# Performance work log

Measured on AMD Instinct MI355X. Metric: run time of the kernel, lower is better.

Reference implementation:

```python
import jax, jax.numpy as jnp
import numpy as np
from jax import lax

B, H, W = 8, 500, 500
M = 2048          # per-image cap on active bottleneck voxels (ragged -> fixed)
GRID = 125        # bottleneck grid size
ENC_RANGE = 125.0
HEADS, ATTN_CH, CH = 4, 128, 64
EPS = 1e-5
NEG = -1e9

def _conv(x, w, b, stride, pad):
    y = lax.conv_general_dilated(x, w, (stride, stride), pad,
                                 dimension_numbers=('NCHW', 'HWIO', 'NCHW'))
    return y + b[None, :, None, None]

def _maxpool2(m):
    return lax.reduce_window(m, -jnp.inf, lax.max, (1, 1, 2, 2), (1, 1, 2, 2), 'VALID')

def setup_inputs():
    key = jax.random.key(0)
    ks = jax.random.split(key, 12)
    occ = (jax.random.uniform(ks[0], (B, 1, H, W)) < 0.005).astype(jnp.float32)
    x = jax.random.normal(ks[1], (B, 1, H, W), dtype=jnp.float32) * occ
    def rn(k, shape, scale):
        return jax.random.normal(k, shape, dtype=jnp.float32) * scale
    return {
        'x': x,
        'w0': rn(ks[2], (3, 3, 1, 32), 0.3), 'b0': jnp.zeros(32, jnp.float32),
        'g0': jnp.ones(32, jnp.float32), 'be0': jnp.zeros(32, jnp.float32),
        'w1': rn(ks[3], (2, 2, 32, 64), 0.1), 'b1': jnp.zeros(64, jnp.float32),
        'g1': jnp.ones(64, jnp.float32), 'be1': jnp.zeros(64, jnp.float32),
        'w2': rn(ks[4], (2, 2, 64, 64), 0.08), 'b2': jnp.zeros(64, jnp.float32),
        'g2': jnp.ones(64, jnp.float32), 'be2': jnp.zeros(64, jnp.float32),
        'wpe': rn(ks[5], (2, 2, CH), 0.5), 'bpe': jnp.zeros((2, CH), jnp.float32),
        'wq': rn(ks[6], (2, CH, ATTN_CH), 0.12), 'bq': jnp.zeros((2, ATTN_CH), jnp.float32),
        'wk': rn(ks[7], (2, CH, ATTN_CH), 0.12), 'bk': jnp.zeros((2, ATTN_CH), jnp.float32),
        'wv': rn(ks[8], (2, CH, ATTN_CH), 0.12), 'bv': jnp.zeros((2, ATTN_CH), jnp.float32),
        'wo': rn(ks[9], (2, ATTN_CH, CH), 0.09), 'bo': jnp.zeros((2, CH), jnp.float32),
        'wh': rn(ks[10], (CH, 4), 0.12), 'bh': jnp.zeros(4, jnp.float32),
    }

def reference(x, w0, b0, g0, be0, w1, b1, g1, be1, w2, b2, g2, be2,
              wpe, bpe, wq, bq, wk, bk, wv, bv, wo, bo, wh, bh):
    # active-site mask (Voxels.from_dense)
    mask0 = (x != 0).any(axis=1, keepdims=True).astype(x.dtype)   # [B,1,500,500]

    def bn_relu(y, g, be):
        # eval-mode BatchNorm1d over active voxel features (running stats 0/1)
        return jax.nn.relu(g[None, :, None, None] * y / jnp.sqrt(1.0 + EPS)
                           + be[None, :, None, None])

    # enc0: submanifold 3x3/s1 -> active set unchanged; inactive inputs are zero
    y = bn_relu(_conv(x, w0, b0, 1, 'SAME'), g0, be0) * mask0
    # enc1/enc2: strided 2x2/s2 -> output active iff any input in window active
    mask1 = _maxpool2(mask0)
    y = bn_relu(_conv(y, w1, b1, 2, 'VALID'), g1, be1) * mask1
    mask2 = _maxpool2(mask1)
    y = bn_relu(_conv(y, w2, b2, 2, 'VALID'), g2, be2) * mask2    # [B,64,125,125]

    # gather active bottleneck voxels per image (ragged -> fixed M + validity mask)
    mflat = mask2.reshape(B, GRID * GRID)
    vals, idx = lax.top_k(mflat, M)     # active-first; stable tie-break (lowest idx)
    valid = vals                        # [B,M] in {0,1}
    feats = jnp.take_along_axis(
        y.reshape(B, CH, GRID * GRID).transpose(0, 2, 1),
        idx[:, :, None], axis=1)        # [B,M,64]
    pos = jnp.stack([idx // GRID, idx % GRID], axis=-1).astype(x.dtype) / ENC_RANGE

    dh = ATTN_CH // HEADS
    kmask = (1.0 - valid)[:, None, None, :] * NEG
    for i in range(2):  # N_ATTN structurally distinct layers
        pe = pos @ wpe[i] + bpe[i]
        h = feats + pe
        q = (h @ wq[i] + bq[i]).reshape(B, M, HEADS, dh)
        k = (h @ wk[i] + bk[i]).reshape(B, M, HEADS, dh)
        v = (h @ wv[i] + bv[i]).reshape(B, M, HEADS, dh)
        s = jnp.einsum('bqhd,bkhd->bhqk', q, k) / jnp.sqrt(jnp.asarray(dh, x.dtype))
        a = jax.nn.softmax(s + kmask, axis=-1)
        o = jnp.einsum('bhqk,bkhd->bqhd', a, v).reshape(B, M, ATTN_CH)
        feats = (feats + o @ wo[i] + bo[i]) * valid[..., None]

    # sparse_global_avg_pool: mean over active voxels per image
    counts = jnp.clip(valid.sum(axis=1, keepdims=True), 1.0, None)
    pooled = feats.sum(axis=1) / counts                            # [B,64]
    return pooled @ wh + bh                                        # [B,4]
```

## Files before the change

kernel.cpp:

```cpp
#include <hip/hip_runtime.h>

#define BDIM   8
#define NPIX   250000
#define G1N    62500
#define G2N    15625
#define NB0    977
#define NB1    245
#define NB2    62
#define CAP0   4096
#define CAP1   4096
#define CAPM   2048
#define CH     64
#define ACH    128
#define NHEADS 4
#define DH     32
#define KSPLIT 4

static constexpr float BN_INV    = 0.99999500003749969f;
static constexpr float ATT_SCALE = 0.17677669529663687f;

typedef _Float16 f16x8 __attribute__((ext_vector_type(8)));
typedef float f32x4 __attribute__((ext_vector_type(4)));

static constexpr size_t E_MAP0  = 0;
static constexpr size_t E_MAP1  = E_MAP0 + (size_t)BDIM*NPIX;
static constexpr size_t E_CNT   = E_MAP1 + (size_t)BDIM*G1N;
static constexpr size_t E_ZEND  = E_CNT + 32;
static constexpr size_t E_BC    = E_ZEND;
static constexpr size_t E_BO    = E_BC + (size_t)3*BDIM*1024;
static constexpr size_t E_BM    = E_BO + (size_t)3*BDIM*1024;
static constexpr size_t E_LIST0 = E_BM + (size_t)3*BDIM*1024*8;
static constexpr size_t E_LIST1 = E_LIST0 + (size_t)BDIM*CAP0;
static constexpr size_t E_LIST2 = E_LIST1 + (size_t)BDIM*CAP1;
static constexpr size_t E_Y0    = E_LIST2 + (size_t)BDIM*CAPM;
static constexpr size_t E_Y1    = E_Y0 + (size_t)BDIM*CAP0*32;
static constexpr size_t E_FE    = E_Y1 + (size_t)BDIM*CAP1*64;
static constexpr size_t E_QF    = E_FE + (size_t)BDIM*CAPM*64;
static constexpr size_t E_KF    = E_QF + (size_t)32*CAPM*32/2;
static constexpr size_t E_VT    = E_KF + (size_t)32*CAPM*32/2;
static constexpr size_t E_PACC  = E_VT + (size_t)32*CAPM*32/2;
static constexpr size_t E_PML   = E_PACC + (size_t)32*CAPM*KSPLIT*32;


__device__ __forceinline__ bool act0(const float* x, int pix, int b) {
  return (pix < NPIX) && (x[(size_t)b * NPIX + pix] != 0.f);
}
__device__ __forceinline__ bool act1(const int* map0, int p, int b) {
  if (p >= G1N) return false;
  int i = p / 250, j = p - i * 250;
  const int* m = map0 + (size_t)b * NPIX + (2 * i) * 500 + 2 * j;
  return (m[0] | m[1] | m[500] | m[501]) != 0;
}
__device__ __forceinline__ bool act2(const int* map1, int p, int b) {
  if (p >= G2N) return false;
  int i = p / 125, j = p - i * 125;
  const int* m = map1 + (size_t)b * G1N + (2 * i) * 250 + 2 * j;
  return (m[0] | m[1] | m[250] | m[251]) != 0;
}

#define COUNT_BODY(ACT_EXPR)                                            \
  int idx = blockIdx.x * 256 + threadIdx.x;                             \
  int b = blockIdx.y;                                                   \
  bool act = (ACT_EXPR);                                                \
  unsigned long long mask = __ballot(act);                              \
  __shared__ int wc[4];                                                 \
  if ((threadIdx.x & 63) == 0) {                                        \
    wc[threadIdx.x >> 6] = __popcll(mask);                              \
    bm[((size_t)b * 1024 + blockIdx.x) * 4 + (threadIdx.x >> 6)] = mask;\
  }                                                                     \
  __syncthreads();                                                      \
  if (threadIdx.x == 0)                                                 \
    bcnt[b * 1024 + blockIdx.x] = wc[0] + wc[1] + wc[2] + wc[3];

__global__ void k_cnt0(const float* __restrict__ x, int* __restrict__ bcnt,
                       unsigned long long* __restrict__ bm) {
  COUNT_BODY(act0(x, idx, b))
}
__global__ void k_cnt1(const int* __restrict__ map0, int* __restrict__ bcnt,
                       unsigned long long* __restrict__ bm) {
  COUNT_BODY(act1(map0, idx, b))
}
__global__ void k_cnt2(const int* __restrict__ map1, int* __restrict__ bcnt,
                       unsigned long long* __restrict__ bm) {
  COUNT_BODY(act2(map1, idx, b))
}

__global__ __launch_bounds__(256) void k_scan(const int* __restrict__ bcnt,
                                              int* __restrict__ boff,
                                              int* __restrict__ cnt,
                                              int nblk, int cbase) {
  int b = blockIdx.x;
  int t = threadIdx.x;
  int base = t * 4;
  int v[4];
  int ts = 0;
#pragma unroll
  for (int u = 0; u < 4; ++u) {
    v[u] = (base + u < nblk) ? bcnt[b * 1024 + base + u] : 0;
    ts += v[u];
  }
  int lane = t & 63, w = t >> 6;
  int incl = ts;
#pragma unroll
  for (int off = 1; off < 64; off <<= 1) {
    int o = __shfl_up(incl, off, 64);
    if (lane >= off) incl += o;
  }
  __shared__ int wsum[4];
  if (lane == 63) wsum[w] = incl;
  __syncthreads();
  int woff = 0;
#pragma unroll
  for (int k = 0; k < 3; ++k) if (k < w) woff += wsum[k];
  int run = woff + incl - ts;
#pragma unroll
  for (int u = 0; u < 4; ++u) {
    if (base + u < nblk) boff[b * 1024 + base + u] = run;
    run += v[u];
  }
  if (t == 255) cnt[cbase + b] = run;
}

#define EMIT_PROLOG                                                     \
  int idx = blockIdx.x * 256 + threadIdx.x;                             \
  int b = blockIdx.y;                                                   \
  int lane = threadIdx.x & 63;                                          \
  unsigned long long mask =                                             \
      bm[((size_t)b * 1024 + blockIdx.x) * 4 + (threadIdx.x >> 6)];     \
  bool act = (mask >> lane) & 1;                                        \
  __shared__ int wbase[4];                                              \
  if (lane == 0) wbase[threadIdx.x >> 6] = __popcll(mask);              \
  __syncthreads();                                                      \
  if (threadIdx.x == 0) {                                               \
    int s = boff[b * 1024 + blockIdx.x];                                \
    for (int w = 0; w < 4; ++w) { int c = wbase[w]; wbase[w] = s; s += c; } \
  }                                                                     \
  __syncthreads();                                                      \
  int slot = wbase[threadIdx.x >> 6] + __popcll(mask & ((1ull << lane) - 1ull));

__global__ void k_emit0(const unsigned long long* __restrict__ bm,
                        const int* __restrict__ boff,
                        int* __restrict__ map0, int* __restrict__ list0) {
  EMIT_PROLOG
  if (act && slot < CAP0) {
    list0[b * CAP0 + slot] = idx;
    map0[(size_t)b * NPIX + idx] = slot + 1;
  }
}
__global__ void k_emit1(const unsigned long long* __restrict__ bm,
                        const int* __restrict__ boff,
                        int* __restrict__ map1, int* __restrict__ list1) {
  EMIT_PROLOG
  if (act && slot < CAP1) {
    list1[b * CAP1 + slot] = idx;
    map1[(size_t)b * G1N + idx] = slot + 1;
  }
}
__global__ void k_emit2(const unsigned long long* __restrict__ bm,
                        const int* __restrict__ boff,
                        int* __restrict__ list2) {
  EMIT_PROLOG
  if (act && slot < CAPM) list2[b * CAPM + slot] = idx;
}


__global__ void k_y0(const float* __restrict__ x, const float* __restrict__ w0,
                     const float* __restrict__ b0, const float* __restrict__ g0,
                     const float* __restrict__ be0,
                     const int* __restrict__ list0, const int* __restrict__ cnt,
                     float* __restrict__ y0) {
  int t = blockIdx.x * 256 + threadIdx.x;
  int b = t >> 17;
  int r = t & 131071;
  int slot = r >> 5, c = r & 31;
  int n = min(cnt[b], CAP0);
  if (slot >= n) return;
  int pix = list0[b * CAP0 + slot];
  int i = pix / 500, j = pix - i * 500;
  float acc = b0[c];
#pragma unroll
  for (int di = 0; di < 3; ++di) {
    int ii = i + di - 1;
    if ((unsigned)ii >= 500u) continue;
#pragma unroll
    for (int dj = 0; dj < 3; ++dj) {
      int jj = j + dj - 1;
      if ((unsigned)jj >= 500u) continue;
      acc += x[(size_t)b * NPIX + ii * 500 + jj] * w0[(di * 3 + dj) * 32 + c];
    }
  }
  float o = g0[c] * acc * BN_INV + be0[c];
  y0[((size_t)(b * CAP0) + slot) * 32 + c] = fmaxf(o, 0.f);
}

__global__ void k_y1(const float* __restrict__ y0, const float* __restrict__ w1,
                     const float* __restrict__ b1, const float* __restrict__ g1,
                     const float* __restrict__ be1,
                     const int* __restrict__ map0, const int* __restrict__ list1,
                     const int* __restrict__ cnt, float* __restrict__ y1) {
  int b = blockIdx.x >> 9;
  int sblk = blockIdx.x & 511;
  int s0 = sblk * 8;
  int n = min(cnt[BDIM + b], CAP1);
  if (s0 >= n) return;
  __shared__ float inT[4][32][8];
  for (int idx = threadIdx.x; idx < 1024; idx += 64) {
    int s = idx & 7;
    int r = idx >> 3;
    int ci = r & 31, pp = r >> 5;
    float v = 0.f;
    int sg = s0 + s;
    if (sg < n) {
      int p = list1[b * CAP1 + sg];
      int i = p / 250, j = p - i * 250;
      int sm = map0[(size_t)b * NPIX + (2 * i + (pp >> 1)) * 500 + (2 * j + (pp & 1))];
      if (sm) v = y0[((size_t)(b * CAP0) + (sm - 1)) * 32 + ci];
    }
    inT[pp][ci][s] = v;
  }
  __syncthreads();
  int co = threadIdx.x;
  float acc[8];
#pragma unroll
  for (int s = 0; s < 8; ++s) acc[s] = b1[co];
#pragma unroll 2
  for (int pp = 0; pp < 4; ++pp)
    for (int ci = 0; ci < 32; ++ci) {
      float wv = w1[((pp << 5) + ci) * 64 + co];
      float4 i0 = *(const float4*)&inT[pp][ci][0];
      float4 i1 = *(const float4*)&inT[pp][ci][4];
      acc[0] += i0.x * wv; acc[1] += i0.y * wv; acc[2] += i0.z * wv; acc[3] += i0.w * wv;
      acc[4] += i1.x * wv; acc[5] += i1.y * wv; acc[6] += i1.z * wv; acc[7] += i1.w * wv;
    }
  int smax = min(8, n - s0);
  for (int s = 0; s < smax; ++s) {
    float o = g1[co] * acc[s] * BN_INV + be1[co];
    y1[((size_t)(b * CAP1) + s0 + s) * 64 + co] = fmaxf(o, 0.f);
  }
}

__global__ void k_y2(const float* __restrict__ y1, const float* __restrict__ w2,
                     const float* __restrict__ b2, const float* __restrict__ g2,
                     const float* __restrict__ be2,
                     const int* __restrict__ map1, const int* __restrict__ list2,
                     const int* __restrict__ cnt, float* __restrict__ feats) {
  int b = blockIdx.x >> 8;
  int sblk = blockIdx.x & 255;
  int s0 = sblk * 8;
  int n = min(cnt[2 * BDIM + b], CAPM);
  if (s0 >= n) return;
  __shared__ float inT[4][64][8];
  for (int idx = threadIdx.x; idx < 2048; idx += 64) {
    int s = idx & 7;
    int r = idx >> 3;
    int ci = r & 63, pp = r >> 6;
    float v = 0.f;
    int sg = s0 + s;
    if (sg < n) {
      int p = list2[b * CAPM + sg];
      int i = p / 125, j = p - i * 125;
      int sm = map1[(size_t)b * G1N + (2 * i + (pp >> 1)) * 250 + (2 * j + (pp & 1))];
      if (sm) v = y1[((size_t)(b * CAP1) + (sm - 1)) * 64 + ci];
    }
    inT[pp][ci][s] = v;
  }
  __syncthreads();
  int co = threadIdx.x;
  float acc[8];
#pragma unroll
  for (int s = 0; s < 8; ++s) acc[s] = b2[co];
#pragma unroll 2
  for (int pp = 0; pp < 4; ++pp)
    for (int ci = 0; ci < 64; ++ci) {
      float wv = w2[((pp << 6) + ci) * 64 + co];
      float4 i0 = *(const float4*)&inT[pp][ci][0];
      float4 i1 = *(const float4*)&inT[pp][ci][4];
      acc[0] += i0.x * wv; acc[1] += i0.y * wv; acc[2] += i0.z * wv; acc[3] += i0.w * wv;
      acc[4] += i1.x * wv; acc[5] += i1.y * wv; acc[6] += i1.z * wv; acc[7] += i1.w * wv;
    }
  int smax = min(8, n - s0);
  for (int s = 0; s < smax; ++s) {
    float o = g2[co] * acc[s] * BN_INV + be2[co];
    feats[((size_t)(b * CAPM) + s0 + s) * 64 + co] = fmaxf(o, 0.f);
  }
}


__global__ void k_qkv(const float* __restrict__ feats, const int* __restrict__ list2,
                      const int* __restrict__ cnt,
                      const float* __restrict__ wpe, const float* __restrict__ bpe,
                      const float* __restrict__ wq, const float* __restrict__ bq,
                      const float* __restrict__ wk, const float* __restrict__ bk,
                      const float* __restrict__ wv, const float* __restrict__ bv,
                      int layer, _Float16* __restrict__ qf, _Float16* __restrict__ kf,
                      _Float16* __restrict__ vt) {
  int b = blockIdx.x & 7;
  int sblk = blockIdx.x >> 3;
  int s0 = sblk * 8;
  int n = min(cnt[2 * BDIM + b], CAPM);
  if (s0 >= n) return;
  __shared__ float hT[64][8];
  for (int idx = threadIdx.x; idx < 512; idx += 128) {
    int s = idx & 7, c = idx >> 3;
    float hv = 0.f;
    int sg = s0 + s;
    if (sg < n) {
      int p = list2[b * CAPM + sg];
      int i = p / 125, j = p - i * 125;
      hv = feats[((size_t)(b * CAPM) + sg) * 64 + c]
         + (float)i * (1.f / 125.f) * wpe[(layer * 2 + 0) * 64 + c]
         + (float)j * (1.f / 125.f) * wpe[(layer * 2 + 1) * 64 + c]
         + bpe[layer * 64 + c];
    }
    hT[c][s] = hv;
  }
  __syncthreads();
  int o = threadIdx.x;
  float accq[8], acck[8], accv[8];
  float bqv = bq[layer * 128 + o], bkv = bk[layer * 128 + o], bvv = bv[layer * 128 + o];
#pragma unroll
  for (int s = 0; s < 8; ++s) { accq[s] = bqv; acck[s] = bkv; accv[s] = bvv; }
  const float* wq_ = wq + (size_t)layer * 64 * 128 + o;
  const float* wk_ = wk + (size_t)layer * 64 * 128 + o;
  const float* wv_ = wv + (size_t)layer * 64 * 128 + o;
  for (int c = 0; c < 64; ++c) {
    float wqv = wq_[c * 128], wkv = wk_[c * 128], wvv = wv_[c * 128];
    float4 h0 = *(const float4*)&hT[c][0];
    float4 h1 = *(const float4*)&hT[c][4];
    float hh[8] = {h0.x, h0.y, h0.z, h0.w, h1.x, h1.y, h1.z, h1.w};
#pragma unroll
    for (int s = 0; s < 8; ++s) {
      accq[s] += hh[s] * wqv; acck[s] += hh[s] * wkv; accv[s] += hh[s] * wvv;
    }
  }
  int hd = o >> 5, d = o & 31;
  size_t bh = (size_t)(b * NHEADS + hd);
  int smax = min(8, n - s0);
  for (int s = 0; s < smax; ++s) {
    size_t rb = (bh * CAPM + s0 + s) * 32 + d;
    qf[rb] = (_Float16)accq[s];
    kf[rb] = (_Float16)acck[s];
    vt[(bh * 32 + d) * CAPM + s0 + s] = (_Float16)accv[s];
  }
}


union U4H8 { uint4 u; f16x8 h; };
union PKU  { _Float16 h[2]; unsigned int u; };

#define LOADK(K0, K1, K2, K3, T0)                                          \
  K0 = *(const f16x8*)(kf + (bh + (T0) + qr) * 32 + g8);                   \
  K1 = *(const f16x8*)(kf + (bh + (T0) + 16 + qr) * 32 + g8);              \
  K2 = *(const f16x8*)(kf + (bh + (T0) + 32 + qr) * 32 + g8);              \
  K3 = *(const f16x8*)(kf + (bh + (T0) + 48 + qr) * 32 + g8);

#define LOADV(V0, V1, V2, V3, T0)                                          \
  V0 = *(const f16x8*)(vbase + (size_t)qr * CAPM + (T0) + g8);             \
  V1 = *(const f16x8*)(vbase + (size_t)(16 + qr) * CAPM + (T0) + g8);      \
  V2 = *(const f16x8*)(vbase + (size_t)qr * CAPM + (T0) + 32 + g8);        \
  V3 = *(const f16x8*)(vbase + (size_t)(16 + qr) * CAPM + (T0) + 32 + g8);

#define PROCESS(K0, K1, K2, K3, V0, V1, V2, V3, T0)                        \
  {                                                                        \
    f32x4 z = {0.f, 0.f, 0.f, 0.f};                                        \
    f32x4 st0 = __builtin_amdgcn_mfma_f32_16x16x32_f16(K0, fq, z, 0, 0, 0);\
    f32x4 st1 = __builtin_amdgcn_mfma_f32_16x16x32_f16(K1, fq, z, 0, 0, 0);\
    f32x4 st2 = __builtin_amdgcn_mfma_f32_16x16x32_f16(K2, fq, z, 0, 0, 0);\
    f32x4 st3 = __builtin_amdgcn_mfma_f32_16x16x32_f16(K3, fq, z, 0, 0, 0);\
    if ((T0) + 64 > n) {                                                   \
      _Pragma("unroll") for (int r = 0; r < 4; ++r) {                      \
        if ((T0) + 4 * g + r >= n)      st0[r] = -1e30f;                   \
        if ((T0) + 16 + 4 * g + r >= n) st1[r] = -1e30f;                   \
        if ((T0) + 32 + 4 * g + r >= n) st2[r] = -1e30f;                   \
        if ((T0) + 48 + 4 * g + r >= n) st3[r] = -1e30f;                   \
      }                                                                    \
    }                                                                      \
    float tm = st0[0];                                                     \
    _Pragma("unroll") for (int r = 1; r < 4; ++r) tm = fmaxf(tm, st0[r]);  \
    _Pragma("unroll") for (int r = 0; r < 4; ++r) tm = fmaxf(tm, st1[r]);  \
    _Pragma("unroll") for (int r = 0; r < 4; ++r) tm = fmaxf(tm, st2[r]);  \
    _Pragma("unroll") for (int r = 0; r < 4; ++r) tm = fmaxf(tm, st3[r]);  \
    tm = fmaxf(tm, __shfl_xor(tm, 16));                                    \
    tm = fmaxf(tm, __shfl_xor(tm, 32));                                    \
    float mn = fmaxf(m, tm * ATT_SCALE);                                   \
    float f_ = __expf(m - mn);                                             \
    m = mn;                                                                \
    float ls = 0.f;                                                        \
    {                                                                      \
      PKU a, c;                                                            \
      a.h[0] = (_Float16)__expf(st0[0] * ATT_SCALE - mn);                  \
      a.h[1] = (_Float16)__expf(st0[1] * ATT_SCALE - mn);                  \
      c.h[0] = (_Float16)__expf(st0[2] * ATT_SCALE - mn);                  \
      c.h[1] = (_Float16)__expf(st0[3] * ATT_SCALE - mn);                  \
      ls += (float)a.h[0] + (float)a.h[1] + (float)c.h[0] + (float)c.h[1]; \
      P[(qr * 32 + 0 + 2 * g) ^ swz] = a.u;                                \
      P[(qr * 32 + 1 + 2 * g) ^ swz] = c.u;                                \
      a.h[0] = (_Float16)__expf(st1[0] * ATT_SCALE - mn);                  \
      a.h[1] = (_Float16)__expf(st1[1] * ATT_SCALE - mn);                  \
      c.h[0] = (_Float16)__expf(st1[2] * ATT_SCALE - mn);                  \
      c.h[1] = (_Float16)__expf(st1[3] * ATT_SCALE - mn);                  \
      ls += (float)a.h[0] + (float)a.h[1] + (float)c.h[0] + (float)c.h[1]; \
      P[(qr * 32 + 8 + 2 * g) ^ swz] = a.u;                                \
      P[(qr * 32 + 9 + 2 * g) ^ swz] = c.u;                                \
      a.h[0] = (_Float16)__expf(st2[0] * ATT_SCALE - mn);                  \
      a.h[1] = (_Float16)__expf(st2[1] * ATT_SCALE - mn);                  \
      c.h[0] = (_Float16)__expf(st2[2] * ATT_SCALE - mn);                  \
      c.h[1] = (_Float16)__expf(st2[3] * ATT_SCALE - mn);                  \
      ls += (float)a.h[0] + (float)a.h[1] + (float)c.h[0] + (float)c.h[1]; \
      P[(qr * 32 + 16 + 2 * g) ^ swz] = a.u;                               \
      P[(qr * 32 + 17 + 2 * g) ^ swz] = c.u;                               \
      a.h[0] = (_Float16)__expf(st3[0] * ATT_SCALE - mn);                  \
      a.h[1] = (_Float16)__expf(st3[1] * ATT_SCALE - mn);                  \
      c.h[0] = (_Float16)__expf(st3[2] * ATT_SCALE - mn);                  \
      c.h[1] = (_Float16)__expf(st3[3] * ATT_SCALE - mn);                  \
      ls += (float)a.h[0] + (float)a.h[1] + (float)c.h[0] + (float)c.h[1]; \
      P[(qr * 32 + 24 + 2 * g) ^ swz] = a.u;                               \
      P[(qr * 32 + 25 + 2 * g) ^ swz] = c.u;                               \
    }                                                                      \
    l = l * f_ + ls;                                                       \
    __builtin_amdgcn_sched_barrier(0);                                     \
    U4H8 pa0, pa1;                                                         \
    pa0.u = *(const uint4*)&P[(qr * 32 + 4 * g) ^ swz];                    \
    pa1.u = *(const uint4*)&P[(qr * 32 + 16 + 4 * g) ^ swz];               \
    acc0[0] *= f_; acc0[1] *= f_; acc0[2] *= f_; acc0[3] *= f_;            \
    acc1[0] *= f_; acc1[1] *= f_; acc1[2] *= f_; acc1[3] *= f_;            \
    acc0 = __builtin_amdgcn_mfma_f32_16x16x32_f16(V0, pa0.h, acc0, 0, 0, 0);\
    acc1 = __builtin_amdgcn_mfma_f32_16x16x32_f16(V1, pa0.h, acc1, 0, 0, 0);\
    acc0 = __builtin_amdgcn_mfma_f32_16x16x32_f16(V2, pa1.h, acc0, 0, 0, 0);\
    acc1 = __builtin_amdgcn_mfma_f32_16x16x32_f16(V3, pa1.h, acc1, 0, 0, 0);\
  }

__global__ __launch_bounds__(64, 4) void k_attn(
    const _Float16* __restrict__ qf, const _Float16* __restrict__ kf,
    const _Float16* __restrict__ vt, const int* __restrict__ cnt,
    float* __restrict__ pacc, float* __restrict__ pml) {
  int b  = blockIdx.x & 7;
  int rr = blockIdx.x >> 3;
  int qt = rr & 127;
  rr >>= 7;
  int h  = rr & 3;
  int ks = rr >> 2;
  int n = min(cnt[2 * BDIM + b], CAPM);
  int q0 = qt * 16;
  if (q0 >= n) return;
  int lane = threadIdx.x;
  int g = lane >> 4, qr = lane & 15;
  int g8 = g * 8;
  size_t bh = (size_t)(b * NHEADS + h) * CAPM;
  const _Float16* vbase = vt + (size_t)(b * NHEADS + h) * 32 * CAPM;
  f16x8 fq = *(const f16x8*)(qf + (bh + q0 + qr) * 32 + g8);
  f32x4 acc0 = {0.f, 0.f, 0.f, 0.f}, acc1 = {0.f, 0.f, 0.f, 0.f};
  float m = -1e30f, l = 0.f;
  __shared__ unsigned int P[512];
  int swz = (qr & 7) << 2;

  int nt = (n + 63) >> 6;
  int tpc = (nt + KSPLIT - 1) / KSPLIT;
  int tb = ks * tpc, te = min(nt, tb + tpc);
  if (tb < te) {
    f16x8 ka0, ka1, ka2, ka3, va0, va1, va2, va3;
    f16x8 kb0, kb1, kb2, kb3, vb0, vb1, vb2, vb3;
    LOADK(ka0, ka1, ka2, ka3, tb * 64)
    LOADV(va0, va1, va2, va3, tb * 64)
    for (int t = tb; t < te; t += 2) {
      if (t + 1 < te) {
        LOADK(kb0, kb1, kb2, kb3, (t + 1) * 64)
        LOADV(vb0, vb1, vb2, vb3, (t + 1) * 64)
      }
      PROCESS(ka0, ka1, ka2, ka3, va0, va1, va2, va3, t * 64)
      if (t + 1 < te) {
        if (t + 2 < te) {
          LOADK(ka0, ka1, ka2, ka3, (t + 2) * 64)
          LOADV(va0, va1, va2, va3, (t + 2) * 64)
        }
        PROCESS(kb0, kb1, kb2, kb3, vb0, vb1, vb2, vb3, (t + 1) * 64)
      }
    }
  }
  l += __shfl_xor(l, 16);
  l += __shfl_xor(l, 32);
  int tok = q0 + qr;
  if (tok < n) {
    float* pp = pacc + ((bh + tok) * KSPLIT + ks) * 32;
#pragma unroll
    for (int r = 0; r < 4; ++r) {
      pp[4 * g + r] = acc0[r];
      pp[16 + 4 * g + r] = acc1[r];
    }
    if (g == 0) {
      float* pm = pml + ((bh + tok) * KSPLIT + ks) * 2;
      pm[0] = m; pm[1] = l;
    }
  }
}


__global__ __launch_bounds__(256) void k_cproj(
    const float* __restrict__ pacc, const float* __restrict__ pml,
    const float* __restrict__ wo, const float* __restrict__ bo,
    const int* __restrict__ cnt, int layer, float* __restrict__ feats) {
  int b = blockIdx.x & 7;
  int sblk = blockIdx.x >> 3;
  int s0 = sblk * 4;
  int n = min(cnt[2 * BDIM + b], CAPM);
  if (s0 >= n) return;
  __shared__ float oT[128][4];
  __shared__ float wgt[4][4][4];
  __shared__ float invL[4][4];
  int t = threadIdx.x;
  if (t < 16) {
    int s = t >> 2, h = t & 3;
    const float* pm = pml + (((size_t)(b * NHEADS + h) * CAPM + s0 + s) * KSPLIT) * 2;
    float m0 = pm[0], l0 = pm[1];
    float m1 = pm[2], l1 = pm[3];
    float m2 = pm[4], l2 = pm[5];
    float m3 = pm[6], l3 = pm[7];
    float M = fmaxf(fmaxf(m0, m1), fmaxf(m2, m3));
    float w0_ = __expf(m0 - M), w1_ = __expf(m1 - M);
    float w2_ = __expf(m2 - M), w3_ = __expf(m3 - M);
    float L = w0_ * l0 + w1_ * l1 + w2_ * l2 + w3_ * l3;
    wgt[s][h][0] = w0_; wgt[s][h][1] = w1_;
    wgt[s][h][2] = w2_; wgt[s][h][3] = w3_;
    invL[s][h] = 1.f / L;
  }
  __syncthreads();
#pragma unroll
  for (int k = 0; k < 2; ++k) {
    int id = t + k * 256;
    int c = id >> 2, s = id & 3;
    int h = c >> 5, d = c & 31;
    const float* pp = pacc + (((size_t)(b * NHEADS + h) * CAPM + s0 + s) * KSPLIT) * 32 + d;
    float v = pp[0]  * wgt[s][h][0] + pp[32] * wgt[s][h][1]
            + pp[64] * wgt[s][h][2] + pp[96] * wgt[s][h][3];
    oT[c][s] = v * invL[s][h];
  }
  __syncthreads();
  int s = t >> 6, co = t & 63;
  float acc = bo[layer * 64 + co];
  const float* w = wo + (size_t)layer * 128 * 64 + co;
#pragma unroll 8
  for (int c = 0; c < 128; ++c) acc += oT[c][s] * w[c * 64];
  int tok = s0 + s;
  if (tok < n) feats[((size_t)(b * CAPM) + tok) * 64 + co] += acc;
}


__global__ __launch_bounds__(1024) void k_head(
    const float* __restrict__ feats, const float* __restrict__ wh,
    const float* __restrict__ bhd, const int* __restrict__ cnt,
    float* __restrict__ out) {
  int b = blockIdx.x;
  int n = min(cnt[2 * BDIM + b], CAPM);
  int c = threadIdx.x & 63, chunk = threadIdx.x >> 6;
  int lo = chunk * 128, hi = min(n, lo + 128);
  float s = 0.f;
  for (int mm = lo; mm < hi; ++mm)
    s += feats[((size_t)(b * CAPM) + mm) * 64 + c];
  __shared__ float red[16][64];
  __shared__ float pooled[64];
  red[chunk][c] = s;
  __syncthreads();
  if (threadIdx.x < 64) {
    float tot = 0.f;
#pragma unroll
    for (int k = 0; k < 16; ++k) tot += red[k][c];
    pooled[c] = tot / (float)max(n, 1);
  }
  __syncthreads();
  if (threadIdx.x < 4) {
    float o = bhd[threadIdx.x];
#pragma unroll
    for (int c2 = 0; c2 < 64; ++c2) o += pooled[c2] * wh[c2 * 4 + threadIdx.x];
    out[b * 4 + threadIdx.x] = o;
  }
}


extern "C" void kernel_launch(void* const* d_in, const int* in_sizes, int n_in,
                              void* d_out, int out_size, void* d_ws, size_t ws_size,
                              hipStream_t stream) {
  const float* x   = (const float*)d_in[0];
  const float* w0  = (const float*)d_in[1];
  const float* b0  = (const float*)d_in[2];
  const float* g0  = (const float*)d_in[3];
  const float* be0 = (const float*)d_in[4];
  const float* w1  = (const float*)d_in[5];
  const float* b1  = (const float*)d_in[6];
  const float* g1  = (const float*)d_in[7];
  const float* be1 = (const float*)d_in[8];
  const float* w2  = (const float*)d_in[9];
  const float* b2  = (const float*)d_in[10];
  const float* g2  = (const float*)d_in[11];
  const float* be2 = (const float*)d_in[12];
  const float* wpe = (const float*)d_in[13];
  const float* bpe = (const float*)d_in[14];
  const float* wq  = (const float*)d_in[15];
  const float* bq  = (const float*)d_in[16];
  const float* wk  = (const float*)d_in[17];
  const float* bk  = (const float*)d_in[18];
  const float* wv  = (const float*)d_in[19];
  const float* bv  = (const float*)d_in[20];
  const float* wo  = (const float*)d_in[21];
  const float* bo  = (const float*)d_in[22];
  const float* wh  = (const float*)d_in[23];
  const float* bh  = (const float*)d_in[24];

  int* wsI = (int*)d_ws;
  float* wsF = (float*)d_ws;
  unsigned long long* bm = (unsigned long long*)(wsI + E_BM);
  _Float16* qf = (_Float16*)(wsI + E_QF);
  _Float16* kf = (_Float16*)(wsI + E_KF);
  _Float16* vt = (_Float16*)(wsI + E_VT);

  hipMemsetAsync(d_ws, 0, E_ZEND * 4, stream);

  k_cnt0<<<dim3(NB0, BDIM), 256, 0, stream>>>(x, wsI + E_BC + 0 * BDIM * 1024,
                                              bm + 0 * BDIM * 4096);
  k_scan<<<BDIM, 256, 0, stream>>>(wsI + E_BC + 0 * BDIM * 1024,
                                   wsI + E_BO + 0 * BDIM * 1024,
                                   wsI + E_CNT, NB0, 0);
  k_emit0<<<dim3(NB0, BDIM), 256, 0, stream>>>(bm + 0 * BDIM * 4096,
                                               wsI + E_BO + 0 * BDIM * 1024,
                                               wsI + E_MAP0, wsI + E_LIST0);
  k_y0<<<(BDIM * CAP0 * 32) / 256, 256, 0, stream>>>(
      x, w0, b0, g0, be0, wsI + E_LIST0, wsI + E_CNT, wsF + E_Y0);
  k_cnt1<<<dim3(NB1, BDIM), 256, 0, stream>>>(wsI + E_MAP0,
                                              wsI + E_BC + 1 * BDIM * 1024,
                                              bm + 1 * BDIM * 4096);
  k_scan<<<BDIM, 256, 0, stream>>>(wsI + E_BC + 1 * BDIM * 1024,
                                   wsI + E_BO + 1 * BDIM * 1024,
                                   wsI + E_CNT, NB1, BDIM);
  k_emit1<<<dim3(NB1, BDIM), 256, 0, stream>>>(bm + 1 * BDIM * 4096,
                                               wsI + E_BO + 1 * BDIM * 1024,
                                               wsI + E_MAP1, wsI + E_LIST1);
  k_y1<<<BDIM * (CAP1 / 8), 64, 0, stream>>>(
      wsF + E_Y0, w1, b1, g1, be1, wsI + E_MAP0, wsI + E_LIST1, wsI + E_CNT, wsF + E_Y1);
  k_cnt2<<<dim3(NB2, BDIM), 256, 0, stream>>>(wsI + E_MAP1,
                                              wsI + E_BC + 2 * BDIM * 1024,
                                              bm + 2 * BDIM * 4096);
  k_scan<<<BDIM, 256, 0, stream>>>(wsI + E_BC + 2 * BDIM * 1024,
                                   wsI + E_BO + 2 * BDIM * 1024,
                                   wsI + E_CNT, NB2, 2 * BDIM);
  k_emit2<<<dim3(NB2, BDIM), 256, 0, stream>>>(bm + 2 * BDIM * 4096,
                                               wsI + E_BO + 2 * BDIM * 1024,
                                               wsI + E_LIST2);
  k_y2<<<BDIM * (CAPM / 8), 64, 0, stream>>>(
      wsF + E_Y1, w2, b2, g2, be2, wsI + E_MAP1, wsI + E_LIST2, wsI + E_CNT, wsF + E_FE);

  for (int layer = 0; layer < 2; ++layer) {
    k_qkv<<<BDIM * (CAPM / 8), 128, 0, stream>>>(
        wsF + E_FE, wsI + E_LIST2, wsI + E_CNT, wpe, bpe, wq, bq, wk, bk, wv, bv,
        layer, qf, kf, vt);
    k_attn<<<BDIM * NHEADS * (CAPM / 16) * KSPLIT, 64, 0, stream>>>(
        qf, kf, vt, wsI + E_CNT, wsF + E_PACC, wsF + E_PML);
    k_cproj<<<BDIM * (CAPM / 4), 256, 0, stream>>>(
        wsF + E_PACC, wsF + E_PML, wo, bo, wsI + E_CNT, layer, wsF + E_FE);
  }

  k_head<<<BDIM, 1024, 0, stream>>>(wsF + E_FE, wh, bh, wsI + E_CNT, (float*)d_out);
}
```

Before: 260.9 us.

## Merge split-K attention partials in-block and widen conv/qkv blocks

The attention kernel now runs its four key-splits as four wavefronts of a single 256-thread block. The partial accumulators and max/sum values are combined in shared memory, and a normalized fp16 output is written directly, so the global pacc/pml round trip and the merge work in the projection kernel go away. Separately, k_y1, k_y2 and k_qkv pack several independent 8-row sub-tiles into each larger block, which cuts the block count. The costs are more shared memory per block and a block-wide barrier. Narrowing the attention output to fp16 before projection can also change precision slightly.

```diff
diff --git a/kernel.cpp b/kernel.cpp
--- a/kernel.cpp
+++ b/kernel.cpp
@@ -38,8 +38,7 @@
 static constexpr size_t E_QF    = E_FE + (size_t)BDIM*CAPM*64;
 static constexpr size_t E_KF    = E_QF + (size_t)32*CAPM*32/2;
 static constexpr size_t E_VT    = E_KF + (size_t)32*CAPM*32/2;
-static constexpr size_t E_PACC  = E_VT + (size_t)32*CAPM*32/2;
-static constexpr size_t E_PML   = E_PACC + (size_t)32*CAPM*KSPLIT*32;
+static constexpr size_t E_O     = E_VT + (size_t)32*CAPM*32/2;
 
 
 __device__ __forceinline__ bool act0(const float* x, int pix, int b) {
@@ -193,18 +192,21 @@
   y0[((size_t)(b * CAP0) + slot) * 32 + c] = fmaxf(o, 0.f);
 }
 
-__global__ void k_y1(const float* __restrict__ y0, const float* __restrict__ w1,
-                     const float* __restrict__ b1, const float* __restrict__ g1,
-                     const float* __restrict__ be1,
-                     const int* __restrict__ map0, const int* __restrict__ list1,
-                     const int* __restrict__ cnt, float* __restrict__ y1) {
-  int b = blockIdx.x >> 9;
-  int sblk = blockIdx.x & 511;
-  int s0 = sblk * 8;
+__global__ __launch_bounds__(256) void k_y1(
+    const float* __restrict__ y0, const float* __restrict__ w1,
+    const float* __restrict__ b1, const float* __restrict__ g1,
+    const float* __restrict__ be1,
+    const int* __restrict__ map0, const int* __restrict__ list1,
+    const int* __restrict__ cnt, float* __restrict__ y1) {
+  int b = blockIdx.x & 7;
+  int qblk = blockIdx.x >> 3;
+  int sub = threadIdx.x >> 6;
+  int co = threadIdx.x & 63;
   int n = min(cnt[BDIM + b], CAP1);
-  if (s0 >= n) return;
-  __shared__ float inT[4][32][8];
-  for (int idx = threadIdx.x; idx < 1024; idx += 64) {
+  if (qblk * 32 >= n) return;
+  int s0 = qblk * 32 + sub * 8;
+  __shared__ float inT[4][4][32][8];
+  for (int idx = co; idx < 1024; idx += 64) {
     int s = idx & 7;
     int r = idx >> 3;
     int ci = r & 31, pp = r >> 5;
@@ -216,10 +218,9 @@
       int sm = map0[(size_t)b * NPIX + (2 * i + (pp >> 1)) * 500 + (2 * j + (pp & 1))];
       if (sm) v = y0[((size_t)(b * CAP0) + (sm - 1)) * 32 + ci];
     }
-    inT[pp][ci][s] = v;
-  }
-  __syncthreads();
-  int co = threadIdx.x;
+    inT[sub][pp][ci][s] = v;
+  }
+  __syncthreads();
   float acc[8];
 #pragma unroll
   for (int s = 0; s < 8; ++s) acc[s] = b1[co];
@@ -227,8 +228,8 @@
   for (int pp = 0; pp < 4; ++pp)
     for (int ci = 0; ci < 32; ++ci) {
       float wv = w1[((pp << 5) + ci) * 64 + co];
-      float4 i0 = *(const float4*)&inT[pp][ci][0];
-      float4 i1 = *(const float4*)&inT[pp][ci][4];
+      float4 i0 = *(const float4*)&inT[sub][pp][ci][0];
+      float4 i1 = *(const float4*)&inT[sub][pp][ci][4];
       acc[0] += i0.x * wv; acc[1] += i0.y * wv; acc[2] += i0.z * wv; acc[3] += i0.w * wv;
       acc[4] += i1.x * wv; acc[5] += i1.y * wv; acc[6] += i1.z * wv; acc[7] += i1.w * wv;
     }
@@ -239,18 +240,21 @@
   }
 }
 
-__global__ void k_y2(const float* __restrict__ y1, const float* __restrict__ w2,
-                     const float* __restrict__ b2, const float* __restrict__ g2,
-                     const float* __restrict__ be2,
-                     const int* __restrict__ map1, const int* __restrict__ list2,
-                     const int* __restrict__ cnt, float* __restrict__ feats) {
-  int b = blockIdx.x >> 8;
-  int sblk = blockIdx.x & 255;
-  int s0 = sblk * 8;
+__global__ __launch_bounds__(256) void k_y2(
+    const float* __restrict__ y1, const float* __restrict__ w2,
+    const float* __restrict__ b2, const float* __restrict__ g2,
+    const float* __restrict__ be2,
+    const int* __restrict__ map1, const int* __restrict__ list2,
+    const int* __restrict__ cnt, float* __restrict__ feats) {
+  int b = blockIdx.x & 7;
+  int qblk = blockIdx.x >> 3;
+  int sub = threadIdx.x >> 6;
+  int co = threadIdx.x & 63;
   int n = min(cnt[2 * BDIM + b], CAPM);
-  if (s0 >= n) return;
-  __shared__ float inT[4][64][8];
-  for (int idx = threadIdx.x; idx < 2048; idx += 64) {
+  if (qblk * 32 >= n) return;
+  int s0 = qblk * 32 + sub * 8;
+  __shared__ float inT[4][4][64][8];
+  for (int idx = co; idx < 2048; idx += 64) {
     int s = idx & 7;
     int r = idx >> 3;
     int ci = r & 63, pp = r >> 6;
@@ -262,10 +266,9 @@
       int sm = map1[(size_t)b * G1N + (2 * i + (pp >> 1)) * 250 + (2 * j + (pp & 1))];
       if (sm) v = y1[((size_t)(b * CAP1) + (sm - 1)) * 64 + ci];
     }
-    inT[pp][ci][s] = v;
-  }
-  __syncthreads();
-  int co = threadIdx.x;
+    inT[sub][pp][ci][s] = v;
+  }
+  __syncthreads();
   float acc[8];
 #pragma unroll
   for (int s = 0; s < 8; ++s) acc[s] = b2[co];
@@ -273,8 +276,8 @@
   for (int pp = 0; pp < 4; ++pp)
     for (int ci = 0; ci < 64; ++ci) {
       float wv = w2[((pp << 6) + ci) * 64 + co];
-      float4 i0 = *(const float4*)&inT[pp][ci][0];
-      float4 i1 = *(const float4*)&inT[pp][ci][4];
+      float4 i0 = *(const float4*)&inT[sub][pp][ci][0];
+      float4 i1 = *(const float4*)&inT[sub][pp][ci][4];
       acc[0] += i0.x * wv; acc[1] += i0.y * wv; acc[2] += i0.z * wv; acc[3] += i0.w * wv;
       acc[4] += i1.x * wv; acc[5] += i1.y * wv; acc[6] += i1.z * wv; acc[7] += i1.w * wv;
     }
@@ -286,21 +289,24 @@
 }
 
 
-__global__ void k_qkv(const float* __restrict__ feats, const int* __restrict__ list2,
-                      const int* __restrict__ cnt,
-                      const float* __restrict__ wpe, const float* __restrict__ bpe,
-                      const float* __restrict__ wq, const float* __restrict__ bq,
-                      const float* __restrict__ wk, const float* __restrict__ bk,
-                      const float* __restrict__ wv, const float* __restrict__ bv,
-                      int layer, _Float16* __restrict__ qf, _Float16* __restrict__ kf,
-                      _Float16* __restrict__ vt) {
+__global__ __launch_bounds__(256) void k_qkv(
+    const float* __restrict__ feats, const int* __restrict__ list2,
+    const int* __restrict__ cnt,
+    const float* __restrict__ wpe, const float* __restrict__ bpe,
+    const float* __restrict__ wq, const float* __restrict__ bq,
+    const float* __restrict__ wk, const float* __restrict__ bk,
+    const float* __restrict__ wv, const float* __restrict__ bv,
+    int layer, _Float16* __restrict__ qf, _Float16* __restrict__ kf,
+    _Float16* __restrict__ vt) {
   int b = blockIdx.x & 7;
-  int sblk = blockIdx.x >> 3;
-  int s0 = sblk * 8;
+  int qblk = blockIdx.x >> 3;
+  int sub = threadIdx.x >> 7;
+  int o = threadIdx.x & 127;
   int n = min(cnt[2 * BDIM + b], CAPM);
-  if (s0 >= n) return;
-  __shared__ float hT[64][8];
-  for (int idx = threadIdx.x; idx < 512; idx += 128) {
+  if (qblk * 16 >= n) return;
+  int s0 = qblk * 16 + sub * 8;
+  __shared__ float hT[2][64][8];
+  for (int idx = o; idx < 512; idx += 128) {
     int s = idx & 7, c = idx >> 3;
     float hv = 0.f;
     int sg = s0 + s;
@@ -312,10 +318,9 @@
          + (float)j * (1.f / 125.f) * wpe[(layer * 2 + 1) * 64 + c]
          + bpe[layer * 64 + c];
     }
-    hT[c][s] = hv;
-  }
-  __syncthreads();
-  int o = threadIdx.x;
+    hT[sub][c][s] = hv;
+  }
+  __syncthreads();
   float accq[8], acck[8], accv[8];
   float bqv = bq[layer * 128 + o], bkv = bk[layer * 128 + o], bvv = bv[layer * 128 + o];
 #pragma unroll
@@ -325,8 +330,8 @@
   const float* wv_ = wv + (size_t)layer * 64 * 128 + o;
   for (int c = 0; c < 64; ++c) {
     float wqv = wq_[c * 128], wkv = wk_[c * 128], wvv = wv_[c * 128];
-    float4 h0 = *(const float4*)&hT[c][0];
-    float4 h1 = *(const float4*)&hT[c][4];
+    float4 h0 = *(const float4*)&hT[sub][c][0];
+    float4 h1 = *(const float4*)&hT[sub][c][4];
     float hh[8] = {h0.x, h0.y, h0.z, h0.w, h1.x, h1.y, h1.z, h1.w};
 #pragma unroll
     for (int s = 0; s < 8; ++s) {
@@ -430,20 +435,19 @@
     acc1 = __builtin_amdgcn_mfma_f32_16x16x32_f16(V3, pa1.h, acc1, 0, 0, 0);\
   }
 
-__global__ __launch_bounds__(64, 4) void k_attn(
+__global__ __launch_bounds__(256) void k_attn(
     const _Float16* __restrict__ qf, const _Float16* __restrict__ kf,
     const _Float16* __restrict__ vt, const int* __restrict__ cnt,
-    float* __restrict__ pacc, float* __restrict__ pml) {
+    _Float16* __restrict__ obuf) {
   int b  = blockIdx.x & 7;
   int rr = blockIdx.x >> 3;
   int qt = rr & 127;
-  rr >>= 7;
-  int h  = rr & 3;
-  int ks = rr >> 2;
+  int h  = rr >> 7;
   int n = min(cnt[2 * BDIM + b], CAPM);
   int q0 = qt * 16;
   if (q0 >= n) return;
-  int lane = threadIdx.x;
+  int ks = threadIdx.x >> 6;
+  int lane = threadIdx.x & 63;
   int g = lane >> 4, qr = lane & 15;
   int g8 = g * 8;
   size_t bh = (size_t)(b * NHEADS + h) * CAPM;
@@ -451,7 +455,10 @@
   f16x8 fq = *(const f16x8*)(qf + (bh + q0 + qr) * 32 + g8);
   f32x4 acc0 = {0.f, 0.f, 0.f, 0.f}, acc1 = {0.f, 0.f, 0.f, 0.f};
   float m = -1e30f, l = 0.f;
-  __shared__ unsigned int P[512];
+  __shared__ unsigned int P4[4][512];
+  __shared__ float partA[4][16][33];
+  __shared__ float mlA[4][16][2];
+  unsigned int* P = P4[ks];
   int swz = (qr & 7) << 2;
 
   int nt = (n + 63) >> 6;
@@ -479,60 +486,54 @@
   }
   l += __shfl_xor(l, 16);
   l += __shfl_xor(l, 32);
-  int tok = q0 + qr;
+#pragma unroll
+  for (int r = 0; r < 4; ++r) {
+    partA[ks][qr][4 * g + r] = acc0[r];
+    partA[ks][qr][16 + 4 * g + r] = acc1[r];
+  }
+  if (g == 0) { mlA[ks][qr][0] = m; mlA[ks][qr][1] = l; }
+  __syncthreads();
+  int t = threadIdx.x;
+  int s = t >> 4;
+  int c0 = (t & 15) * 2;
+  int tok = q0 + s;
   if (tok < n) {
-    float* pp = pacc + ((bh + tok) * KSPLIT + ks) * 32;
-#pragma unroll
-    for (int r = 0; r < 4; ++r) {
-      pp[4 * g + r] = acc0[r];
-      pp[16 + 4 * g + r] = acc1[r];
-    }
-    if (g == 0) {
-      float* pm = pml + ((bh + tok) * KSPLIT + ks) * 2;
-      pm[0] = m; pm[1] = l;
-    }
-  }
-}
-
-
-__global__ __launch_bounds__(256) void k_cproj(
-    const float* __restrict__ pacc, const float* __restrict__ pml,
-    const float* __restrict__ wo, const float* __restrict__ bo,
-    const int* __restrict__ cnt, int layer, float* __restrict__ feats) {
+    float m0 = mlA[0][s][0], l0 = mlA[0][s][1];
+    float m1 = mlA[1][s][0], l1 = mlA[1][s][1];
+    float m2 = mlA[2][s][0], l2 = mlA[2][s][1];
+    float m3 = mlA[3][s][0], l3 = mlA[3][s][1];
+    float M = fmaxf(fmaxf(m0, m1), fmaxf(m2, m3));
+    float w0_ = __expf(m0 - M), w1_ = __expf(m1 - M);
+    float w2_ = __expf(m2 - M), w3_ = __expf(m3 - M);
+    float invL = 1.f / (w0_ * l0 + w1_ * l1 + w2_ * l2 + w3_ * l3);
+    float v0 = (partA[0][s][c0] * w0_ + partA[1][s][c0] * w1_ +
+                partA[2][s][c0] * w2_ + partA[3][s][c0] * w3_) * invL;
+    float v1 = (partA[0][s][c0 + 1] * w0_ + partA[1][s][c0 + 1] * w1_ +
+                partA[2][s][c0 + 1] * w2_ + partA[3][s][c0 + 1] * w3_) * invL;
+    _Float16* op = obuf + ((size_t)b * CAPM + tok) * ACH + h * DH;
+    op[c0] = (_Float16)v0;
+    op[c0 + 1] = (_Float16)v1;
+  }
+}
+
+
+__global__ __launch_bounds__(256) void k_proj(
+    const _Float16* __restrict__ obuf, const float* __restrict__ wo,
+    const float* __restrict__ bo, const int* __restrict__ cnt,
+    int layer, float* __restrict__ feats) {
   int b = blockIdx.x & 7;
   int sblk = blockIdx.x >> 3;
   int s0 = sblk * 4;
   int n = min(cnt[2 * BDIM + b], CAPM);
   if (s0 >= n) return;
   __shared__ float oT[128][4];
-  __shared__ float wgt[4][4][4];
-  __shared__ float invL[4][4];
   int t = threadIdx.x;
-  if (t < 16) {
-    int s = t >> 2, h = t & 3;
-    const float* pm = pml + (((size_t)(b * NHEADS + h) * CAPM + s0 + s) * KSPLIT) * 2;
-    float m0 = pm[0], l0 = pm[1];
-    float m1 = pm[2], l1 = pm[3];
-    float m2 = pm[4], l2 = pm[5];
-    float m3 = pm[6], l3 = pm[7];
-    float M = fmaxf(fmaxf(m0, m1), fmaxf(m2, m3));
-    float w0_ = __expf(m0 - M), w1_ = __expf(m1 - M);
-    float w2_ = __expf(m2 - M), w3_ = __expf(m3 - M);
-    float L = w0_ * l0 + w1_ * l1 + w2_ * l2 + w3_ * l3;
-    wgt[s][h][0] = w0_; wgt[s][h][1] = w1_;
-    wgt[s][h][2] = w2_; wgt[s][h][3] = w3_;
-    invL[s][h] = 1.f / L;
-  }
-  __syncthreads();
 #pragma unroll
   for (int k = 0; k < 2; ++k) {
     int id = t + k * 256;
     int c = id >> 2, s = id & 3;
-    int h = c >> 5, d = c & 31;
-    const float* pp = pacc + (((size_t)(b * NHEADS + h) * CAPM + s0 + s) * KSPLIT) * 32 + d;
-    float v = pp[0]  * wgt[s][h][0] + pp[32] * wgt[s][h][1]
-            + pp[64] * wgt[s][h][2] + pp[96] * wgt[s][h][3];
-    oT[c][s] = v * invL[s][h];
+    int sg = s0 + s;
+    oT[c][s] = (sg < n) ? (float)obuf[((size_t)b * CAPM + sg) * ACH + c] : 0.f;
   }
   __syncthreads();
   int s = t >> 6, co = t & 63;
@@ -611,6 +612,7 @@
   _Float16* qf = (_Float16*)(wsI + E_QF);
   _Float16* kf = (_Float16*)(wsI + E_KF);
   _Float16* vt = (_Float16*)(wsI + E_VT);
+  _Float16* ob = (_Float16*)(wsI + E_O);
 
   hipMemsetAsync(d_ws, 0, E_ZEND * 4, stream);
 
@@ -633,7 +635,7 @@
   k_emit1<<<dim3(NB1, BDIM), 256, 0, stream>>>(bm + 1 * BDIM * 4096,
                                                wsI + E_BO + 1 * BDIM * 1024,
                                                wsI + E_MAP1, wsI + E_LIST1);
-  k_y1<<<BDIM * (CAP1 / 8), 64, 0, stream>>>(
+  k_y1<<<BDIM * (CAP1 / 32), 256, 0, stream>>>(
       wsF + E_Y0, w1, b1, g1, be1, wsI + E_MAP0, wsI + E_LIST1, wsI + E_CNT, wsF + E_Y1);
   k_cnt2<<<dim3(NB2, BDIM), 256, 0, stream>>>(wsI + E_MAP1,
                                               wsI + E_BC + 2 * BDIM * 1024,
@@ -644,17 +646,17 @@
   k_emit2<<<dim3(NB2, BDIM), 256, 0, stream>>>(bm + 2 * BDIM * 4096,
                                                wsI + E_BO + 2 * BDIM * 1024,
                                                wsI + E_LIST2);
-  k_y2<<<BDIM * (CAPM / 8), 64, 0, stream>>>(
+  k_y2<<<BDIM * (CAPM / 32), 256, 0, stream>>>(
       wsF + E_Y1, w2, b2, g2, be2, wsI + E_MAP1, wsI + E_LIST2, wsI + E_CNT, wsF + E_FE);
 
   for (int layer = 0; layer < 2; ++layer) {
-    k_qkv<<<BDIM * (CAPM / 8), 128, 0, stream>>>(
+    k_qkv<<<BDIM * (CAPM / 16), 256, 0, stream>>>(
         wsF + E_FE, wsI + E_LIST2, wsI + E_CNT, wpe, bpe, wq, bq, wk, bk, wv, bv,
         layer, qf, kf, vt);
-    k_attn<<<BDIM * NHEADS * (CAPM / 16) * KSPLIT, 64, 0, stream>>>(
-        qf, kf, vt, wsI + E_CNT, wsF + E_PACC, wsF + E_PML);
-    k_cproj<<<BDIM * (CAPM / 4), 256, 0, stream>>>(
-        wsF + E_PACC, wsF + E_PML, wo, bo, wsI + E_CNT, layer, wsF + E_FE);
+    k_attn<<<BDIM * NHEADS * (CAPM / 16), 256, 0, stream>>>(
+        qf, kf, vt, wsI + E_CNT, ob);
+    k_proj<<<BDIM * (CAPM / 4), 256, 0, stream>>>(
+        ob, wo, bo, wsI + E_CNT, layer, wsF + E_FE);
   }
 
   k_head<<<BDIM, 1024, 0, stream>>>(wsF + E_FE, wh, bh, wsI + E_CNT, (float*)d_out);
```

After: 246.7 us. -5.4%, faster.
